# Performance work log

Measured on AMD Instinct MI355X. Metric: run time of the kernel, lower is better.

Reference implementation:

```python
import jax, jax.numpy as jnp
import numpy as np
import math


def setup_inputs() -> dict:
    key = jax.random.key(0)
    k1, k2, k3, k4 = jax.random.split(key, 4)
    B, H, S, D = 4, 16, 2048, 64
    return {
        "query": jax.random.normal(k1, (B, H, S, D), dtype=jnp.float32),
        "key": jax.random.normal(k2, (B, H, S, D), dtype=jnp.float32),
        "value": jax.random.normal(k3, (B, H, S, D), dtype=jnp.float32),
        "mask": jax.random.randint(k4, (B, S), 0, 2, dtype=jnp.int32),
    }


def reference(query, key, value, mask):
    # scores: [B, H, Sq, Skv]
    d = query.shape[-1]
    scores = jnp.einsum("bhqd,bhkd->bhqk", query, key) / math.sqrt(d)
    # torch branch: 2D mask [B, Skv] -> [B, 1, Sq, Skv] (broadcast over heads)
    m = mask[:, None, None, :]  # repeat over Sq is a pure broadcast
    scores = jnp.where(m == 0, jnp.float32(-1e9), scores)
    p_attn = jax.nn.softmax(scores, axis=-1)
    out = jnp.einsum("bhqk,bhkd->bhqd", p_attn, value)
    return out, p_attn
```

## Files before the change

kernel.cpp:

```cpp
#include <hip/hip_runtime.h>

#define SS 2048
#define DD 64
#define TQ 64
#define NCHUNK (SS / 64)
#define LSTR 72

typedef __attribute__((ext_vector_type(8))) short     short8;
typedef __attribute__((ext_vector_type(8))) __bf16    bf16x8;
typedef __attribute__((ext_vector_type(4))) float     float4v;
typedef __attribute__((ext_vector_type(4))) unsigned short ushort4v;

__device__ __forceinline__ unsigned short f2bf(float x) {
    unsigned u = __float_as_uint(x);
    u += 0x7fffu + ((u >> 16) & 1u);
    return (unsigned short)(u >> 16);
}

__device__ __forceinline__ bf16x8 ld_frag(const unsigned short* p) {
    return __builtin_bit_cast(bf16x8, *(const short8*)p);
}

__global__ __launch_bounds__(256, 2) void attn_fused(
    const float* __restrict__ Q, const float* __restrict__ K,
    const float* __restrict__ V, const int* __restrict__ mask,
    float* __restrict__ outp, float* __restrict__ pattn)
{
    __shared__ unsigned short Qs[TQ * LSTR];
    __shared__ unsigned short Ks[64 * LSTR];
    __shared__ unsigned short Vt[64 * LSTR];
    __shared__ unsigned short Pw[4 * 16 * LSTR];
    __shared__ float biasf[64];

    const int tid  = threadIdx.x;
    const int w    = tid >> 6;
    const int lane = tid & 63;
    const int lq   = lane & 15;
    const int quad = lane >> 4;

    const int bh = blockIdx.x;
    const int b  = bh >> 4;
    const int q0 = blockIdx.y * TQ;

    const float* Qg = Q + ((size_t)bh * SS + q0) * DD;
    const float* Kg = K + (size_t)bh * SS * DD;
    const float* Vg = V + (size_t)bh * SS * DD;
    const int*   mg = mask + b * SS;

    #pragma unroll
    for (int it = 0; it < 4; ++it) {
        int e4 = it * 256 + tid;
        int row = e4 >> 4, c4 = e4 & 15;
        float4v v = *(const float4v*)(Qg + e4 * 4);
        ushort4v h;
        h[0] = f2bf(v[0] * 0.125f); h[1] = f2bf(v[1] * 0.125f);
        h[2] = f2bf(v[2] * 0.125f); h[3] = f2bf(v[3] * 0.125f);
        *(ushort4v*)(Qs + row * LSTR + c4 * 4) = h;
    }
    __syncthreads();

    bf16x8 a0 = ld_frag(Qs + (w * 16 + lq) * LSTR + quad * 8);
    bf16x8 a1 = ld_frag(Qs + (w * 16 + lq) * LSTR + 32 + quad * 8);

    float m_r[4], l_r[4];
    #pragma unroll
    for (int r = 0; r < 4; ++r) { m_r[r] = -INFINITY; l_r[r] = 0.0f; }

    for (int c = 0; c < NCHUNK; ++c) {
        __syncthreads();
        const float* Kc = Kg + (size_t)(c * 64) * DD;
        #pragma unroll
        for (int it = 0; it < 4; ++it) {
            int e4 = it * 256 + tid;
            int row = e4 >> 4, c4 = e4 & 15;
            float4v v = *(const float4v*)(Kc + e4 * 4);
            ushort4v h;
            h[0] = f2bf(v[0]); h[1] = f2bf(v[1]); h[2] = f2bf(v[2]); h[3] = f2bf(v[3]);
            *(ushort4v*)(Ks + row * LSTR + c4 * 4) = h;
        }
        if (tid < 64) biasf[tid] = (mg[c * 64 + tid] == 0) ? -1e9f : 0.0f;
        __syncthreads();

        float4v sc[4];
        #pragma unroll
        for (int t = 0; t < 4; ++t) {
            float bias = biasf[t * 16 + lq];
            float4v acc = {bias, bias, bias, bias};
            bf16x8 b0 = ld_frag(Ks + (t * 16 + lq) * LSTR + quad * 8);
            bf16x8 b1 = ld_frag(Ks + (t * 16 + lq) * LSTR + 32 + quad * 8);
            acc = __builtin_amdgcn_mfma_f32_16x16x32_bf16(a0, b0, acc, 0, 0, 0);
            acc = __builtin_amdgcn_mfma_f32_16x16x32_bf16(a1, b1, acc, 0, 0, 0);
            sc[t] = acc;
        }
        #pragma unroll
        for (int r = 0; r < 4; ++r) {
            float mx = fmaxf(fmaxf(sc[0][r], sc[1][r]), fmaxf(sc[2][r], sc[3][r]));
            float mn = fmaxf(m_r[r], mx);
            float sum = __expf(sc[0][r] - mn) + __expf(sc[1][r] - mn)
                      + __expf(sc[2][r] - mn) + __expf(sc[3][r] - mn);
            l_r[r] = l_r[r] * __expf(m_r[r] - mn) + sum;
            m_r[r] = mn;
        }
    }

    #pragma unroll
    for (int r = 0; r < 4; ++r) {
        float m = m_r[r], l = l_r[r];
        #pragma unroll
        for (int off = 1; off < 16; off <<= 1) {
            float mo = __shfl_xor(m, off, 64);
            float lo = __shfl_xor(l, off, 64);
            float mn = fmaxf(m, mo);
            l = l * __expf(m - mn) + lo * __expf(mo - mn);
            m = mn;
        }
        m_r[r] = m;
        l_r[r] = 1.0f / l;
    }

    float4v oacc[4];
    #pragma unroll
    for (int t = 0; t < 4; ++t) oacc[t] = (float4v){0.f, 0.f, 0.f, 0.f};

    unsigned short* pw = Pw + w * 16 * LSTR;

    for (int c = 0; c < NCHUNK; ++c) {
        __syncthreads();
        const float* Kc = Kg + (size_t)(c * 64) * DD;
        const float* Vc = Vg + (size_t)(c * 64) * DD;
        #pragma unroll
        for (int it = 0; it < 4; ++it) {
            int e4 = it * 256 + tid;
            int row = e4 >> 4, c4 = e4 & 15;
            float4v v = *(const float4v*)(Kc + e4 * 4);
            ushort4v h;
            h[0] = f2bf(v[0]); h[1] = f2bf(v[1]); h[2] = f2bf(v[2]); h[3] = f2bf(v[3]);
            *(ushort4v*)(Ks + row * LSTR + c4 * 4) = h;
            float4v vv = *(const float4v*)(Vc + e4 * 4);
            Vt[(c4 * 4 + 0) * LSTR + row] = f2bf(vv[0]);
            Vt[(c4 * 4 + 1) * LSTR + row] = f2bf(vv[1]);
            Vt[(c4 * 4 + 2) * LSTR + row] = f2bf(vv[2]);
            Vt[(c4 * 4 + 3) * LSTR + row] = f2bf(vv[3]);
        }
        if (tid < 64) biasf[tid] = (mg[c * 64 + tid] == 0) ? -1e9f : 0.0f;
        __syncthreads();

        float4v sc[4];
        #pragma unroll
        for (int t = 0; t < 4; ++t) {
            float bias = biasf[t * 16 + lq];
            float4v acc = {bias, bias, bias, bias};
            bf16x8 b0 = ld_frag(Ks + (t * 16 + lq) * LSTR + quad * 8);
            bf16x8 b1 = ld_frag(Ks + (t * 16 + lq) * LSTR + 32 + quad * 8);
            acc = __builtin_amdgcn_mfma_f32_16x16x32_bf16(a0, b0, acc, 0, 0, 0);
            acc = __builtin_amdgcn_mfma_f32_16x16x32_bf16(a1, b1, acc, 0, 0, 0);
            sc[t] = acc;
        }

        float* pg = pattn + ((size_t)bh * SS + (q0 + w * 16 + quad * 4)) * SS + c * 64;
        #pragma unroll
        for (int t = 0; t < 4; ++t) {
            #pragma unroll
            for (int r = 0; r < 4; ++r) {
                float p = __expf(sc[t][r] - m_r[r]) * l_r[r];
                pg[(size_t)r * SS + t * 16 + lq] = p;
                pw[(quad * 4 + r) * LSTR + t * 16 + lq] = f2bf(p);
            }
        }
        __syncthreads();

        #pragma unroll
        for (int ks = 0; ks < 2; ++ks) {
            bf16x8 pa = ld_frag(pw + lq * LSTR + ks * 32 + quad * 8);
            #pragma unroll
            for (int t = 0; t < 4; ++t) {
                bf16x8 vb = ld_frag(Vt + (t * 16 + lq) * LSTR + ks * 32 + quad * 8);
                oacc[t] = __builtin_amdgcn_mfma_f32_16x16x32_bf16(pa, vb, oacc[t], 0, 0, 0);
            }
        }
    }

    float* og = outp + ((size_t)bh * SS + (q0 + w * 16 + quad * 4)) * DD;
    #pragma unroll
    for (int t = 0; t < 4; ++t) {
        #pragma unroll
        for (int r = 0; r < 4; ++r) {
            og[(size_t)r * DD + t * 16 + lq] = oacc[t][r];
        }
    }
}

extern "C" void kernel_launch(void* const* d_in, const int* in_sizes, int n_in,
                              void* d_out, int out_size, void* d_ws, size_t ws_size,
                              hipStream_t stream) {
    const float* Q    = (const float*)d_in[0];
    const float* K    = (const float*)d_in[1];
    const float* V    = (const float*)d_in[2];
    const int*   mask = (const int*)d_in[3];
    float* outp  = (float*)d_out;
    float* pattn = outp + (size_t)4 * 16 * 2048 * 64;

    dim3 grid(64, SS / TQ);
    attn_fused<<<grid, 256, 0, stream>>>(Q, K, V, mask, outp, pattn);
}
```

Before: 1.505 ms.

## Precompute bf16 K and transposed V in a prep kernel; load fragments directly from global

Adds a prep kernel that converts K to bf16 and writes V as a transposed bf16 array into the workspace. The attention kernel then loads MFMA fragments straight from global memory instead of staging K/V through LDS. This removes the per-block redundant fp32-to-bf16 conversion and most __syncthreads barriers. The kernel also drops the Q shared tile, reads the mask bias directly, swizzles the per-wave P buffer, and raises the occupancy hint to 4. The trade-offs are an extra launch, workspace traffic, and uncoalesced 16-byte global fragment loads that rely on L2 hits. The memory-clobber fence stands in for a barrier on the per-wave P buffer, which relies on each wave using only its own region.

```diff
diff --git a/kernel.cpp b/kernel.cpp
--- a/kernel.cpp
+++ b/kernel.cpp
@@ -4,11 +4,10 @@
 #define DD 64
 #define TQ 64
 #define NCHUNK (SS / 64)
-#define LSTR 72
-
-typedef __attribute__((ext_vector_type(8))) short     short8;
-typedef __attribute__((ext_vector_type(8))) __bf16    bf16x8;
-typedef __attribute__((ext_vector_type(4))) float     float4v;
+
+typedef __attribute__((ext_vector_type(8))) short          short8;
+typedef __attribute__((ext_vector_type(8))) __bf16         bf16x8;
+typedef __attribute__((ext_vector_type(4))) float          float4v;
 typedef __attribute__((ext_vector_type(4))) unsigned short ushort4v;
 
 __device__ __forceinline__ unsigned short f2bf(float x) {
@@ -21,16 +20,46 @@
     return __builtin_bit_cast(bf16x8, *(const short8*)p);
 }
 
-__global__ __launch_bounds__(256, 2) void attn_fused(
-    const float* __restrict__ Q, const float* __restrict__ K,
-    const float* __restrict__ V, const int* __restrict__ mask,
+__global__ __launch_bounds__(256) void prep_kv(
+    const float* __restrict__ K, const float* __restrict__ V,
+    unsigned short* __restrict__ Kb, unsigned short* __restrict__ Vtb)
+{
+    const int tid = threadIdx.x;
+    const int bh  = blockIdx.x;
+    const int ch  = blockIdx.y;
+
+    const float* Kc = K + ((size_t)bh * SS + ch * 64) * DD;
+    unsigned short* Kbc = Kb + ((size_t)bh * SS + ch * 64) * DD;
+    #pragma unroll
+    for (int it = 0; it < 4; ++it) {
+        int e4 = it * 256 + tid;
+        float4v v = *(const float4v*)(Kc + e4 * 4);
+        ushort4v h;
+        h[0] = f2bf(v[0]); h[1] = f2bf(v[1]); h[2] = f2bf(v[2]); h[3] = f2bf(v[3]);
+        *(ushort4v*)(Kbc + e4 * 4) = h;
+    }
+
+    const float* Vc = V + ((size_t)bh * SS + ch * 64) * DD;
+    unsigned short* Vtc = Vtb + (size_t)bh * DD * SS + ch * 64;
+    #pragma unroll
+    for (int it = 0; it < 4; ++it) {
+        int e4 = it * 256 + tid;
+        int s  = e4 & 63;
+        int g  = e4 >> 6;
+        float4v v = *(const float4v*)(Vc + s * DD + g * 4);
+        Vtc[(g * 4 + 0) * SS + s] = f2bf(v[0]);
+        Vtc[(g * 4 + 1) * SS + s] = f2bf(v[1]);
+        Vtc[(g * 4 + 2) * SS + s] = f2bf(v[2]);
+        Vtc[(g * 4 + 3) * SS + s] = f2bf(v[3]);
+    }
+}
+
+__global__ __launch_bounds__(256, 4) void attn_fused(
+    const float* __restrict__ Q, const unsigned short* __restrict__ Kb,
+    const unsigned short* __restrict__ Vtb, const int* __restrict__ mask,
     float* __restrict__ outp, float* __restrict__ pattn)
 {
-    __shared__ unsigned short Qs[TQ * LSTR];
-    __shared__ unsigned short Ks[64 * LSTR];
-    __shared__ unsigned short Vt[64 * LSTR];
-    __shared__ unsigned short Pw[4 * 16 * LSTR];
-    __shared__ float biasf[64];
+    __shared__ unsigned short Pw[4 * 16 * 64];
 
     const int tid  = threadIdx.x;
     const int w    = tid >> 6;
@@ -42,54 +71,48 @@
     const int b  = bh >> 4;
     const int q0 = blockIdx.y * TQ;
 
-    const float* Qg = Q + ((size_t)bh * SS + q0) * DD;
-    const float* Kg = K + (size_t)bh * SS * DD;
-    const float* Vg = V + (size_t)bh * SS * DD;
-    const int*   mg = mask + b * SS;
-
-    #pragma unroll
-    for (int it = 0; it < 4; ++it) {
-        int e4 = it * 256 + tid;
-        int row = e4 >> 4, c4 = e4 & 15;
-        float4v v = *(const float4v*)(Qg + e4 * 4);
-        ushort4v h;
-        h[0] = f2bf(v[0] * 0.125f); h[1] = f2bf(v[1] * 0.125f);
-        h[2] = f2bf(v[2] * 0.125f); h[3] = f2bf(v[3] * 0.125f);
-        *(ushort4v*)(Qs + row * LSTR + c4 * 4) = h;
-    }
-    __syncthreads();
-
-    bf16x8 a0 = ld_frag(Qs + (w * 16 + lq) * LSTR + quad * 8);
-    bf16x8 a1 = ld_frag(Qs + (w * 16 + lq) * LSTR + 32 + quad * 8);
+    const unsigned short* Kg = Kb  + (size_t)bh * SS * DD;
+    const unsigned short* Vg = Vtb + (size_t)bh * DD * SS;
+    const int* mg = mask + b * SS;
+
+    bf16x8 a0, a1;
+    {
+        const float* Qg = Q + ((size_t)bh * SS + q0 + w * 16 + lq) * DD + quad * 8;
+        float4v q00 = *(const float4v*)(Qg);
+        float4v q01 = *(const float4v*)(Qg + 4);
+        float4v q10 = *(const float4v*)(Qg + 32);
+        float4v q11 = *(const float4v*)(Qg + 36);
+        short8 s0, s1;
+        #pragma unroll
+        for (int j = 0; j < 4; ++j) {
+            s0[j]     = (short)f2bf(q00[j] * 0.125f);
+            s0[j + 4] = (short)f2bf(q01[j] * 0.125f);
+            s1[j]     = (short)f2bf(q10[j] * 0.125f);
+            s1[j + 4] = (short)f2bf(q11[j] * 0.125f);
+        }
+        a0 = __builtin_bit_cast(bf16x8, s0);
+        a1 = __builtin_bit_cast(bf16x8, s1);
+    }
 
     float m_r[4], l_r[4];
     #pragma unroll
     for (int r = 0; r < 4; ++r) { m_r[r] = -INFINITY; l_r[r] = 0.0f; }
 
     for (int c = 0; c < NCHUNK; ++c) {
-        __syncthreads();
-        const float* Kc = Kg + (size_t)(c * 64) * DD;
-        #pragma unroll
-        for (int it = 0; it < 4; ++it) {
-            int e4 = it * 256 + tid;
-            int row = e4 >> 4, c4 = e4 & 15;
-            float4v v = *(const float4v*)(Kc + e4 * 4);
-            ushort4v h;
-            h[0] = f2bf(v[0]); h[1] = f2bf(v[1]); h[2] = f2bf(v[2]); h[3] = f2bf(v[3]);
-            *(ushort4v*)(Ks + row * LSTR + c4 * 4) = h;
-        }
-        if (tid < 64) biasf[tid] = (mg[c * 64 + tid] == 0) ? -1e9f : 0.0f;
-        __syncthreads();
-
+        const unsigned short* Kc = Kg + (size_t)(c * 64) * DD;
+        bf16x8 kb0[4], kb1[4];
+        #pragma unroll
+        for (int t = 0; t < 4; ++t) {
+            kb0[t] = ld_frag(Kc + (t * 16 + lq) * DD + quad * 8);
+            kb1[t] = ld_frag(Kc + (t * 16 + lq) * DD + 32 + quad * 8);
+        }
         float4v sc[4];
         #pragma unroll
         for (int t = 0; t < 4; ++t) {
-            float bias = biasf[t * 16 + lq];
+            float bias = (mg[c * 64 + t * 16 + lq] == 0) ? -1e9f : 0.0f;
             float4v acc = {bias, bias, bias, bias};
-            bf16x8 b0 = ld_frag(Ks + (t * 16 + lq) * LSTR + quad * 8);
-            bf16x8 b1 = ld_frag(Ks + (t * 16 + lq) * LSTR + 32 + quad * 8);
-            acc = __builtin_amdgcn_mfma_f32_16x16x32_bf16(a0, b0, acc, 0, 0, 0);
-            acc = __builtin_amdgcn_mfma_f32_16x16x32_bf16(a1, b1, acc, 0, 0, 0);
+            acc = __builtin_amdgcn_mfma_f32_16x16x32_bf16(a0, kb0[t], acc, 0, 0, 0);
+            acc = __builtin_amdgcn_mfma_f32_16x16x32_bf16(a1, kb1[t], acc, 0, 0, 0);
             sc[t] = acc;
         }
         #pragma unroll
@@ -122,39 +145,35 @@
     #pragma unroll
     for (int t = 0; t < 4; ++t) oacc[t] = (float4v){0.f, 0.f, 0.f, 0.f};
 
-    unsigned short* pw = Pw + w * 16 * LSTR;
+    unsigned short* pw = Pw + w * 16 * 64;
+    const int rswz = (lq & 7) << 3;
 
     for (int c = 0; c < NCHUNK; ++c) {
-        __syncthreads();
-        const float* Kc = Kg + (size_t)(c * 64) * DD;
-        const float* Vc = Vg + (size_t)(c * 64) * DD;
-        #pragma unroll
-        for (int it = 0; it < 4; ++it) {
-            int e4 = it * 256 + tid;
-            int row = e4 >> 4, c4 = e4 & 15;
-            float4v v = *(const float4v*)(Kc + e4 * 4);
-            ushort4v h;
-            h[0] = f2bf(v[0]); h[1] = f2bf(v[1]); h[2] = f2bf(v[2]); h[3] = f2bf(v[3]);
-            *(ushort4v*)(Ks + row * LSTR + c4 * 4) = h;
-            float4v vv = *(const float4v*)(Vc + e4 * 4);
-            Vt[(c4 * 4 + 0) * LSTR + row] = f2bf(vv[0]);
-            Vt[(c4 * 4 + 1) * LSTR + row] = f2bf(vv[1]);
-            Vt[(c4 * 4 + 2) * LSTR + row] = f2bf(vv[2]);
-            Vt[(c4 * 4 + 3) * LSTR + row] = f2bf(vv[3]);
-        }
-        if (tid < 64) biasf[tid] = (mg[c * 64 + tid] == 0) ? -1e9f : 0.0f;
-        __syncthreads();
-
+        const unsigned short* Kc = Kg + (size_t)(c * 64) * DD;
+        bf16x8 kb0[4], kb1[4];
+        #pragma unroll
+        for (int t = 0; t < 4; ++t) {
+            kb0[t] = ld_frag(Kc + (t * 16 + lq) * DD + quad * 8);
+            kb1[t] = ld_frag(Kc + (t * 16 + lq) * DD + 32 + quad * 8);
+        }
         float4v sc[4];
         #pragma unroll
         for (int t = 0; t < 4; ++t) {
-            float bias = biasf[t * 16 + lq];
+            float bias = (mg[c * 64 + t * 16 + lq] == 0) ? -1e9f : 0.0f;
             float4v acc = {bias, bias, bias, bias};
-            bf16x8 b0 = ld_frag(Ks + (t * 16 + lq) * LSTR + quad * 8);
-            bf16x8 b1 = ld_frag(Ks + (t * 16 + lq) * LSTR + 32 + quad * 8);
-            acc = __builtin_amdgcn_mfma_f32_16x16x32_bf16(a0, b0, acc, 0, 0, 0);
-            acc = __builtin_amdgcn_mfma_f32_16x16x32_bf16(a1, b1, acc, 0, 0, 0);
+            acc = __builtin_amdgcn_mfma_f32_16x16x32_bf16(a0, kb0[t], acc, 0, 0, 0);
+            acc = __builtin_amdgcn_mfma_f32_16x16x32_bf16(a1, kb1[t], acc, 0, 0, 0);
             sc[t] = acc;
+        }
+
+        bf16x8 vb[4][2];
+        #pragma unroll
+        for (int t = 0; t < 4; ++t) {
+            #pragma unroll
+            for (int ks = 0; ks < 2; ++ks) {
+                vb[t][ks] = ld_frag(Vg + (size_t)(t * 16 + lq) * SS
+                                       + c * 64 + ks * 32 + quad * 8);
+            }
         }
 
         float* pg = pattn + ((size_t)bh * SS + (q0 + w * 16 + quad * 4)) * SS + c * 64;
@@ -164,18 +183,18 @@
             for (int r = 0; r < 4; ++r) {
                 float p = __expf(sc[t][r] - m_r[r]) * l_r[r];
                 pg[(size_t)r * SS + t * 16 + lq] = p;
-                pw[(quad * 4 + r) * LSTR + t * 16 + lq] = f2bf(p);
+                int row = quad * 4 + r;
+                pw[row * 64 + ((t * 16 + lq) ^ ((row & 7) << 3))] = f2bf(p);
             }
         }
-        __syncthreads();
+        asm volatile("" ::: "memory");
 
         #pragma unroll
         for (int ks = 0; ks < 2; ++ks) {
-            bf16x8 pa = ld_frag(pw + lq * LSTR + ks * 32 + quad * 8);
+            bf16x8 pa = ld_frag(pw + lq * 64 + ((ks * 32 + quad * 8) ^ rswz));
             #pragma unroll
             for (int t = 0; t < 4; ++t) {
-                bf16x8 vb = ld_frag(Vt + (t * 16 + lq) * LSTR + ks * 32 + quad * 8);
-                oacc[t] = __builtin_amdgcn_mfma_f32_16x16x32_bf16(pa, vb, oacc[t], 0, 0, 0);
+                oacc[t] = __builtin_amdgcn_mfma_f32_16x16x32_bf16(pa, vb[t][ks], oacc[t], 0, 0, 0);
             }
         }
     }
@@ -200,6 +219,12 @@
     float* outp  = (float*)d_out;
     float* pattn = outp + (size_t)4 * 16 * 2048 * 64;
 
+    unsigned short* Kb  = (unsigned short*)d_ws;
+    unsigned short* Vtb = Kb + (size_t)64 * SS * DD;
+
+    dim3 pgrid(64, NCHUNK);
+    prep_kv<<<pgrid, 256, 0, stream>>>(K, V, Kb, Vtb);
+
     dim3 grid(64, SS / TQ);
-    attn_fused<<<grid, 256, 0, stream>>>(Q, K, V, mask, outp, pattn);
-}
+    attn_fused<<<grid, 256, 0, stream>>>(Q, Kb, Vtb, mask, outp, pattn);
+}
```

New measurement: 1.706 ms. +13.4%, slower.
